# Kernel optimization log

Hardware: AMD Instinct MI355X
Metric: run time of the kernel (lower is better)

The kernel has to match this reference:

```python
import jax, jax.numpy as jnp
import numpy as np

B, T, S, H, V = 8, 1024, 1024, 1024, 5000


def setup_inputs() -> dict:
    key = jax.random.key(0)
    ks = jax.random.split(key, 9)
    x = jax.random.normal(ks[0], (B, T, H), dtype=jnp.float32)
    encoder_attn_w = jax.random.uniform(ks[1], (B, T, S), dtype=jnp.float32)
    # normalize like attention weights over source dim
    encoder_attn_w = encoder_attn_w / jnp.sum(encoder_attn_w, axis=-1, keepdims=True)
    nodes = jax.random.randint(ks[2], (B, S), 0, V)
    scale = 0.02
    Wg = jax.random.normal(ks[3], (H, 1), dtype=jnp.float32) * scale
    bg = jnp.zeros((1,), dtype=jnp.float32)
    Wf = jax.random.normal(ks[4], (H, H), dtype=jnp.float32) * scale
    bf = jnp.zeros((H,), dtype=jnp.float32)
    Wv = jax.random.normal(ks[5], (H, V), dtype=jnp.float32) * scale
    bv = jnp.zeros((V,), dtype=jnp.float32)
    return {"x": x, "encoder_attn_w": encoder_attn_w, "nodes": nodes,
            "Wg": Wg, "bg": bg, "Wf": Wf, "bf": bf, "Wv": Wv, "bv": bv}


def reference(x, encoder_attn_w, nodes, Wg, bg, Wf, bf, Wv, bv):
    # Conv1D == affine along last dim (GPT-2 style): x @ W + b
    p_gen = jax.nn.sigmoid(x @ Wg + bg)                      # [B,T,1]
    h = jax.nn.gelu(x @ Wf + bf)                             # fc with activation
    logits = h @ Wv + bv                                     # [B,T,V]
    out = jax.nn.softmax(logits, axis=-1) * p_gen            # gated generate dist
    # pointer/copy: scatter-add attention mass (1 - p_gen) into vocab slots
    add = encoder_attn_w * (1.0 - p_gen)                     # [B,T,S]
    b_idx = jnp.arange(B)[:, None, None]
    t_idx = jnp.arange(T)[None, :, None]
    v_idx = jnp.broadcast_to(nodes[:, None, :], (B, T, S))
    out = out.at[b_idx, t_idx, v_idx].add(add)
    return out
```

## Files before the change

kernel.cpp:

```cpp
#include <hip/hip_runtime.h>

#define Mq   8192
#define Hq   1024
#define Sq   1024
#define Tq   1024
#define Vq   5000
#define Vpad 5120

typedef __bf16 bf16;
typedef bf16  bf16x8 __attribute__((ext_vector_type(8)));
typedef bf16  bf16x4 __attribute__((ext_vector_type(4)));
typedef float f32x4  __attribute__((ext_vector_type(4)));

typedef const __attribute__((address_space(1))) void* gas_t;
typedef __attribute__((address_space(3))) void*       sas_t;

__device__ __forceinline__ void async_copy16(const void* g, void* s) {
  __builtin_amdgcn_global_load_lds((gas_t)g, (sas_t)s, 16, 0, 0);
}

__global__ __launch_bounds__(256) void pgen_cvt(
    const float* __restrict__ x, const float* __restrict__ Wg,
    const float* __restrict__ bg, bf16* __restrict__ xb,
    float* __restrict__ pgen) {
  const int m = blockIdx.x;
  const int t = threadIdx.x;
  float4 v = ((const float4*)(x + (size_t)m * Hq))[t];
  float4 g = ((const float4*)Wg)[t];
  float dot = v.x * g.x + v.y * g.y + v.z * g.z + v.w * g.w;
  bf16x4 o;
  o[0] = (bf16)v.x; o[1] = (bf16)v.y; o[2] = (bf16)v.z; o[3] = (bf16)v.w;
  ((bf16x4*)(xb + (size_t)m * Hq))[t] = o;
  #pragma unroll
  for (int off = 32; off; off >>= 1) dot += __shfl_down(dot, off, 64);
  __shared__ float red[4];
  if ((t & 63) == 0) red[t >> 6] = dot;
  __syncthreads();
  if (t == 0) {
    float s = red[0] + red[1] + red[2] + red[3] + bg[0];
    pgen[m] = 1.0f / (1.0f + __expf(-s));
  }
}

__global__ __launch_bounds__(256) void transpose_cvt(
    const float* __restrict__ W, bf16* __restrict__ WT,
    int K, int Nin, int Npad) {
  __shared__ float tile[32][33];
  const int nb = blockIdx.x * 32, kb = blockIdx.y * 32;
  const int tx = threadIdx.x, ty = threadIdx.y;
  #pragma unroll
  for (int i = 0; i < 32; i += 8) {
    int k = kb + ty + i, n = nb + tx;
    tile[ty + i][tx] = (n < Nin) ? W[(size_t)k * Nin + n] : 0.0f;
  }
  __syncthreads();
  #pragma unroll
  for (int i = 0; i < 32; i += 8) {
    int n = nb + ty + i, k = kb + tx;
    if (n < Npad) WT[(size_t)n * K + k] = (bf16)tile[tx][ty + i];
  }
}

template <int MODE>
__global__ __launch_bounds__(256, 2) void gemm_mfma(
    const bf16* __restrict__ A, const bf16* __restrict__ BT,
    const float* __restrict__ bias, float* __restrict__ outF,
    bf16* __restrict__ outB, int M, int N, int K, int Nstore) {
  __shared__ bf16 As[128 * 32];
  __shared__ bf16 Bs[128 * 32];
  const int tid  = threadIdx.x;
  const int w    = tid >> 6;
  const int l    = tid & 63;
  const int quad = l >> 4;
  const int t16  = l & 15;
  const int wm   = (w >> 1) * 64;
  const int wn   = (w & 1) * 64;
  const int m0   = blockIdx.x * 128;
  const int n0   = blockIdx.y * 128;
  const int srow = l >> 2;
  const int scol = (l & 3) * 8;

  f32x4 acc[4][4] = {};

  for (int k0 = 0; k0 < K; k0 += 32) {
    __syncthreads();
    #pragma unroll
    for (int r = 0; r < 2; ++r) {
      const int chunk = r * 4 + w;
      const int mrow  = chunk * 16 + srow;
      async_copy16(A  + (size_t)(m0 + mrow) * K + k0 + scol, As + chunk * 512);
      async_copy16(BT + (size_t)(n0 + mrow) * K + k0 + scol, Bs + chunk * 512);
    }
    __syncthreads();

    bf16x8 af[4], bfr[4];
    #pragma unroll
    for (int i = 0; i < 4; ++i)
      af[i] = *(const bf16x8*)(As + (wm + 16 * i + t16) * 32 + quad * 8);
    #pragma unroll
    for (int j = 0; j < 4; ++j)
      bfr[j] = *(const bf16x8*)(Bs + (wn + 16 * j + t16) * 32 + quad * 8);
    #pragma unroll
    for (int i = 0; i < 4; ++i)
      #pragma unroll
      for (int j = 0; j < 4; ++j)
        acc[i][j] = __builtin_amdgcn_mfma_f32_16x16x32_bf16(af[i], bfr[j], acc[i][j], 0, 0, 0);
  }

  float bj[4];
  #pragma unroll
  for (int j = 0; j < 4; ++j) {
    const int ng = n0 + wn + 16 * j + t16;
    bj[j] = (MODE == 0 || ng < Nstore) ? bias[ng] : 0.0f;
  }

  #pragma unroll
  for (int i = 0; i < 4; ++i) {
    const int mg = m0 + wm + 16 * i + quad * 4;
    #pragma unroll
    for (int j = 0; j < 4; ++j) {
      const int ng = n0 + wn + 16 * j + t16;
      #pragma unroll
      for (int r = 0; r < 4; ++r) {
        float v = acc[i][j][r] + bj[j];
        if (MODE == 0) {
          float u  = 0.7978845608028654f * (v + 0.044715f * v * v * v);
          float e2 = __expf(2.0f * u);
          float th = 1.0f - 2.0f / (e2 + 1.0f);
          outB[(size_t)(mg + r) * N + ng] = (bf16)(0.5f * v * (1.0f + th));
        } else if (MODE == 1) {
          if (ng < Nstore)
            outB[(size_t)(mg + r) * Nstore + ng] = (bf16)__expf(v);
        } else {
          if (ng < Nstore)
            outF[(size_t)(mg + r) * Nstore + ng] = __expf(v);
        }
      }
    }
  }
}

template <typename ET>
__global__ __launch_bounds__(256) void finalize(
    float* __restrict__ out, const ET* __restrict__ e,
    const float* __restrict__ pgen, const float* __restrict__ attn,
    const int* __restrict__ nodes) {
  const int m = blockIdx.x;
  const int b = m / Tq;
  const int t = threadIdx.x;
  __shared__ float buf[Vq];
  __shared__ float red[4];

  float s = 0.0f;
  const ET* erow = e + (size_t)m * Vq;
  if constexpr (sizeof(ET) == 2) {
    const bf16x8* e8 = (const bf16x8*)erow;
    for (int i = t; i < Vq / 8; i += 256) {
      bf16x8 v = e8[i];
      #pragma unroll
      for (int k = 0; k < 8; ++k) {
        float f = (float)v[k];
        buf[i * 8 + k] = f;
        s += f;
      }
    }
  } else {
    const float4* e4 = (const float4*)erow;
    for (int i = t; i < Vq / 4; i += 256) {
      float4 v = e4[i];
      buf[i * 4 + 0] = v.x; buf[i * 4 + 1] = v.y;
      buf[i * 4 + 2] = v.z; buf[i * 4 + 3] = v.w;
      s += (v.x + v.y) + (v.z + v.w);
    }
  }
  #pragma unroll
  for (int off = 32; off; off >>= 1) s += __shfl_down(s, off, 64);
  if ((t & 63) == 0) red[t >> 6] = s;
  __syncthreads();
  s = red[0] + red[1] + red[2] + red[3];

  const float pg    = pgen[m];
  const float scale = pg / s;
  const float coef  = (1.0f - pg) / scale;

  const float* arow = attn + (size_t)m * Sq;
  const int*   nrow = nodes + (size_t)b * Sq;
  for (int sIdx = t; sIdx < Sq; sIdx += 256)
    atomicAdd(&buf[nrow[sIdx]], arow[sIdx] * coef);
  __syncthreads();

  float4* o4 = (float4*)(out + (size_t)m * Vq);
  const float4* b4 = (const float4*)buf;
  for (int i = t; i < Vq / 4; i += 256) {
    float4 v = b4[i];
    v.x *= scale; v.y *= scale; v.z *= scale; v.w *= scale;
    o4[i] = v;
  }
}

extern "C" void kernel_launch(void* const* d_in, const int* in_sizes, int n_in,
                              void* d_out, int out_size, void* d_ws, size_t ws_size,
                              hipStream_t stream) {
  const float* x    = (const float*)d_in[0];
  const float* attn = (const float*)d_in[1];
  const int*   nodes= (const int*)d_in[2];
  const float* Wg   = (const float*)d_in[3];
  const float* bg   = (const float*)d_in[4];
  const float* Wf   = (const float*)d_in[5];
  const float* bf_  = (const float*)d_in[6];
  const float* Wv   = (const float*)d_in[7];
  const float* bv   = (const float*)d_in[8];
  float* out = (float*)d_out;

  char* w = (char*)d_ws;

  const size_t NEED = 111312896ull;
  const bool big = ws_size >= NEED;

  if (big) {
    bf16*  eB   = (bf16*)(w);
    bf16*  xb   = (bf16*)(w);
    bf16*  hB   = (bf16*)(w + 81920000ull);
    bf16*  WfT  = (bf16*)(w + 98697216ull);
    bf16*  WvT  = (bf16*)(w + 100794368ull);
    float* pgen = (float*)(w + 111280128ull);

    pgen_cvt<<<Mq, 256, 0, stream>>>(x, Wg, bg, xb, pgen);
    transpose_cvt<<<dim3(Hq / 32, Hq / 32), dim3(32, 8), 0, stream>>>(Wf, WfT, Hq, Hq, Hq);
    transpose_cvt<<<dim3(Vpad / 32, Hq / 32), dim3(32, 8), 0, stream>>>(Wv, WvT, Hq, Vq, Vpad);
    gemm_mfma<0><<<dim3(Mq / 128, Hq / 128), 256, 0, stream>>>(
        xb, WfT, bf_, nullptr, hB, Mq, Hq, Hq, Hq);
    gemm_mfma<1><<<dim3(Mq / 128, Vpad / 128), 256, 0, stream>>>(
        hB, WvT, bv, nullptr, eB, Mq, Vpad, Hq, Vq);
    finalize<bf16><<<Mq, 256, 0, stream>>>(out, eB, pgen, attn, nodes);
  } else {
    bf16*  xb   = (bf16*)(w);
    bf16*  hB   = (bf16*)(w + 16777216);
    bf16*  WfT  = (bf16*)(w + 33554432);
    bf16*  WvT  = (bf16*)(w + 35651584);
    float* pgen = (float*)(w + 46137344);

    pgen_cvt<<<Mq, 256, 0, stream>>>(x, Wg, bg, xb, pgen);
    transpose_cvt<<<dim3(Hq / 32, Hq / 32), dim3(32, 8), 0, stream>>>(Wf, WfT, Hq, Hq, Hq);
    transpose_cvt<<<dim3(Vpad / 32, Hq / 32), dim3(32, 8), 0, stream>>>(Wv, WvT, Hq, Vq, Vpad);
    gemm_mfma<0><<<dim3(Mq / 128, Hq / 128), 256, 0, stream>>>(
        xb, WfT, bf_, nullptr, hB, Mq, Hq, Hq, Hq);
    gemm_mfma<2><<<dim3(Mq / 128, Vpad / 128), 256, 0, stream>>>(
        hB, WvT, bv, out, nullptr, Mq, Vpad, Hq, Vq);
    finalize<float><<<Mq, 256, 0, stream>>>(out, out, pgen, attn, nodes);
  }
}
```

Measured before the change: 420.8 us.

## Remap GEMM blocks per XCD for L2 reuse and streamline finalize

The GEMM grid becomes 1D and block IDs are remapped so that each XCD (bid&7) owns a fixed band of N tiles and walks through M. The intent is to keep the same weight columns resident in that XCD's L2 cache. The bf16 finalize now keeps the exp values in registers instead of staging them in shared memory. It scatters raw attention into a zeroed buffer and computes scale*e + (1-pg)*buf on output, which removes a shared-memory pass. The risk is that the fixed mapping assumes round-robin dispatch across 8 XCDs and tile counts divisible by Q.

```diff
diff --git a/kernel.cpp b/kernel.cpp
--- a/kernel.cpp
+++ b/kernel.cpp
@@ -61,13 +61,18 @@
   }
 }
 
-template <int MODE>
+template <int MODE, int Q>
 __global__ __launch_bounds__(256, 2) void gemm_mfma(
     const bf16* __restrict__ A, const bf16* __restrict__ BT,
     const float* __restrict__ bias, float* __restrict__ outF,
     bf16* __restrict__ outB, int M, int N, int K, int Nstore) {
   __shared__ bf16 As[128 * 32];
   __shared__ bf16 Bs[128 * 32];
+  const int bid = blockIdx.x;
+  const int xcd = bid & 7;
+  const int rr  = bid >> 3;
+  const int nb  = xcd * Q + rr % Q;
+  const int mb  = rr / Q;
   const int tid  = threadIdx.x;
   const int w    = tid >> 6;
   const int l    = tid & 63;
@@ -75,8 +80,8 @@
   const int t16  = l & 15;
   const int wm   = (w >> 1) * 64;
   const int wn   = (w & 1) * 64;
-  const int m0   = blockIdx.x * 128;
-  const int n0   = blockIdx.y * 128;
+  const int m0   = mb * 128;
+  const int n0   = nb * 128;
   const int srow = l >> 2;
   const int scol = (l & 3) * 8;
 
@@ -140,9 +145,8 @@
   }
 }
 
-template <typename ET>
-__global__ __launch_bounds__(256) void finalize(
-    float* __restrict__ out, const ET* __restrict__ e,
+__global__ __launch_bounds__(256) void finalize_fast(
+    float* __restrict__ out, const bf16* __restrict__ e,
     const float* __restrict__ pgen, const float* __restrict__ attn,
     const int* __restrict__ nodes) {
   const int m = blockIdx.x;
@@ -151,26 +155,20 @@
   __shared__ float buf[Vq];
   __shared__ float red[4];
 
+  float4* buf4 = (float4*)buf;
+  const float4 z4 = {0.f, 0.f, 0.f, 0.f};
+  for (int i = t; i < Vq / 4; i += 256) buf4[i] = z4;
+
+  const bf16x8* e8 = (const bf16x8*)(e + (size_t)m * Vq);
+  bf16x8 ev[3];
   float s = 0.0f;
-  const ET* erow = e + (size_t)m * Vq;
-  if constexpr (sizeof(ET) == 2) {
-    const bf16x8* e8 = (const bf16x8*)erow;
-    for (int i = t; i < Vq / 8; i += 256) {
-      bf16x8 v = e8[i];
-      #pragma unroll
-      for (int k = 0; k < 8; ++k) {
-        float f = (float)v[k];
-        buf[i * 8 + k] = f;
-        s += f;
-      }
-    }
-  } else {
-    const float4* e4 = (const float4*)erow;
-    for (int i = t; i < Vq / 4; i += 256) {
-      float4 v = e4[i];
-      buf[i * 4 + 0] = v.x; buf[i * 4 + 1] = v.y;
-      buf[i * 4 + 2] = v.z; buf[i * 4 + 3] = v.w;
-      s += (v.x + v.y) + (v.z + v.w);
+  #pragma unroll
+  for (int c = 0; c < 3; ++c) {
+    const int i = t + c * 256;
+    if (i < Vq / 8) {
+      ev[c] = e8[i];
+      #pragma unroll
+      for (int k = 0; k < 8; ++k) s += (float)ev[c][k];
     }
   }
   #pragma unroll
@@ -179,16 +177,63 @@
   __syncthreads();
   s = red[0] + red[1] + red[2] + red[3];
 
+  const float pg    = pgen[m];
+  const float scale = pg / s;
+  const float coefw = 1.0f - pg;
+
+  const float* arow = attn + (size_t)m * Sq;
+  const int*   nrow = nodes + (size_t)b * Sq;
+  for (int sIdx = t; sIdx < Sq; sIdx += 256)
+    atomicAdd(&buf[nrow[sIdx]], arow[sIdx]);
+  __syncthreads();
+
+  float4* o4 = (float4*)(out + (size_t)m * Vq);
+  #pragma unroll
+  for (int c = 0; c < 3; ++c) {
+    const int i = t + c * 256;
+    if (i < Vq / 8) {
+      float f[8];
+      #pragma unroll
+      for (int k = 0; k < 8; ++k)
+        f[k] = (float)ev[c][k] * scale + buf[i * 8 + k] * coefw;
+      float4 lo = {f[0], f[1], f[2], f[3]};
+      float4 hi = {f[4], f[5], f[6], f[7]};
+      o4[i * 2 + 0] = lo;
+      o4[i * 2 + 1] = hi;
+    }
+  }
+}
+
+__global__ __launch_bounds__(256) void finalize_f32(
+    float* __restrict__ out, const float* __restrict__ e,
+    const float* __restrict__ pgen, const float* __restrict__ attn,
+    const int* __restrict__ nodes) {
+  const int m = blockIdx.x;
+  const int b = m / Tq;
+  const int t = threadIdx.x;
+  __shared__ float buf[Vq];
+  __shared__ float red[4];
+  float s = 0.0f;
+  const float4* e4 = (const float4*)(e + (size_t)m * Vq);
+  for (int i = t; i < Vq / 4; i += 256) {
+    float4 v = e4[i];
+    buf[i * 4 + 0] = v.x; buf[i * 4 + 1] = v.y;
+    buf[i * 4 + 2] = v.z; buf[i * 4 + 3] = v.w;
+    s += (v.x + v.y) + (v.z + v.w);
+  }
+  #pragma unroll
+  for (int off = 32; off; off >>= 1) s += __shfl_down(s, off, 64);
+  if ((t & 63) == 0) red[t >> 6] = s;
+  __syncthreads();
+  s = red[0] + red[1] + red[2] + red[3];
   const float pg    = pgen[m];
   const float scale = pg / s;
   const float coef  = (1.0f - pg) / scale;
-
   const float* arow = attn + (size_t)m * Sq;
   const int*   nrow = nodes + (size_t)b * Sq;
   for (int sIdx = t; sIdx < Sq; sIdx += 256)
     atomicAdd(&buf[nrow[sIdx]], arow[sIdx] * coef);
   __syncthreads();
-
   float4* o4 = (float4*)(out + (size_t)m * Vq);
   const float4* b4 = (const float4*)buf;
   for (int i = t; i < Vq / 4; i += 256) {
@@ -213,7 +258,6 @@
   float* out = (float*)d_out;
 
   char* w = (char*)d_ws;
-
   const size_t NEED = 111312896ull;
   const bool big = ws_size >= NEED;
 
@@ -228,11 +272,11 @@
     pgen_cvt<<<Mq, 256, 0, stream>>>(x, Wg, bg, xb, pgen);
     transpose_cvt<<<dim3(Hq / 32, Hq / 32), dim3(32, 8), 0, stream>>>(Wf, WfT, Hq, Hq, Hq);
     transpose_cvt<<<dim3(Vpad / 32, Hq / 32), dim3(32, 8), 0, stream>>>(Wv, WvT, Hq, Vq, Vpad);
-    gemm_mfma<0><<<dim3(Mq / 128, Hq / 128), 256, 0, stream>>>(
+    gemm_mfma<0, 1><<<512, 256, 0, stream>>>(
         xb, WfT, bf_, nullptr, hB, Mq, Hq, Hq, Hq);
-    gemm_mfma<1><<<dim3(Mq / 128, Vpad / 128), 256, 0, stream>>>(
+    gemm_mfma<1, 5><<<2560, 256, 0, stream>>>(
         hB, WvT, bv, nullptr, eB, Mq, Vpad, Hq, Vq);
-    finalize<bf16><<<Mq, 256, 0, stream>>>(out, eB, pgen, attn, nodes);
+    finalize_fast<<<Mq, 256, 0, stream>>>(out, eB, pgen, attn, nodes);
   } else {
     bf16*  xb   = (bf16*)(w);
     bf16*  hB   = (bf16*)(w + 16777216);
@@ -243,10 +287,10 @@
     pgen_cvt<<<Mq, 256, 0, stream>>>(x, Wg, bg, xb, pgen);
     transpose_cvt<<<dim3(Hq / 32, Hq / 32), dim3(32, 8), 0, stream>>>(Wf, WfT, Hq, Hq, Hq);
     transpose_cvt<<<dim3(Vpad / 32, Hq / 32), dim3(32, 8), 0, stream>>>(Wv, WvT, Hq, Vq, Vpad);
-    gemm_mfma<0><<<dim3(Mq / 128, Hq / 128), 256, 0, stream>>>(
+    gemm_mfma<0, 1><<<512, 256, 0, stream>>>(
         xb, WfT, bf_, nullptr, hB, Mq, Hq, Hq, Hq);
-    gemm_mfma<2><<<dim3(Mq / 128, Vpad / 128), 256, 0, stream>>>(
+    gemm_mfma<2, 5><<<2560, 256, 0, stream>>>(
         hB, WvT, bv, out, nullptr, Mq, Vpad, Hq, Vq);
-    finalize<float><<<Mq, 256, 0, stream>>>(out, out, pgen, attn, nodes);
-  }
-}
+    finalize_f32<<<Mq, 256, 0, stream>>>(out, out, pgen, attn, nodes);
+  }
+}
```

After: 429.3 us. 1.02x slower.
